# Optimization experiments

Hardware: AMD Instinct MI355X
Metric: run time of the kernel (lower is better)

Reference implementation:

```python
import jax, jax.numpy as jnp
import numpy as np

N, C_IN, NCLASS, H, W = 4, 32, 2, 64, 64


def setup_inputs() -> dict:
    key = jax.random.key(0)
    k1, k2, k3, k4, k5, k6 = jax.random.split(key, 6)
    return {
        "feature_in": jax.random.normal(k1, (N, C_IN, H, W), dtype=jnp.float32),
        "out": jax.random.normal(k2, (N, NCLASS, H, W), dtype=jnp.float32),
        "w1": jax.random.normal(k3, (NCLASS, C_IN), dtype=jnp.float32) * 0.1,
        "b1": jax.random.normal(k4, (NCLASS,), dtype=jnp.float32) * 0.1,
        "w2": jax.random.normal(k5, (NCLASS, C_IN), dtype=jnp.float32) * 0.1,
        "b2": jax.random.normal(k6, (NCLASS,), dtype=jnp.float32) * 0.1,
    }


def reference(feature_in, out, w1, b1, w2, b2):
    # h_in, w_in == input H, W (ceil(H/1)); bilinear resize to the same size
    # with align_corners=True is an exact identity, so no resampling is needed.
    n, c, h, w = feature_in.shape
    hw = h * w
    out = jax.lax.stop_gradient(out)  # out.detach() in the original

    # 1x1 convs == per-pixel linear projections
    f1 = jnp.einsum('nchw,kc->nkhw', feature_in, w1) + b1[None, :, None, None]
    f2 = jnp.einsum('nchw,kc->nkhw', feature_in, w2) + b2[None, :, None, None]
    f1 = f1.reshape(n, -1, hw)          # n k (h w)
    f2 = f2.reshape(n, -1, hw)
    out_flat = out.reshape(n, -1, hw)   # n c (h w)

    scale = 1.0 / jnp.sqrt(jnp.float32(f1.shape[1]))
    corr_map = jnp.einsum('nkp,nkq->npq', f1, f2) * scale  # [n, hw, hw]
    corr_map = jax.nn.softmax(corr_map, axis=-1)

    o = jnp.einsum('ncp,npq->ncq', out_flat, corr_map)
    return o.reshape(n, -1, h, w)
```

## Files before the change

### kernel.cpp

```cpp
#include <hip/hip_runtime.h>

#define HW   4096
#define CIN  32
#define SCALE2 (0.70710678118654752f * 1.44269504088896340f)

__device__ __forceinline__ float exp2_raw(float x) {
#if __has_builtin(__builtin_amdgcn_exp2f)
    return __builtin_amdgcn_exp2f(x);
#else
    float r;
    asm("v_exp_f32 %0, %1" : "=v"(r) : "v"(x));
    return r;
#endif
}

__global__ __launch_bounds__(256) void proj_kernel(
        const float* __restrict__ feat,
        const float* __restrict__ w1, const float* __restrict__ b1,
        const float* __restrict__ w2, const float* __restrict__ b2,
        float2* __restrict__ f1v, float2* __restrict__ f2v) {
    __shared__ float4 red[4][64];
    int tid = threadIdx.x;
    int pl = tid & 63;
    int cq = tid >> 6;
    int b = blockIdx.x;
    int n = b >> 6;
    int p = ((b & 63) << 6) + pl;
    const float* fbase = feat + ((size_t)n * CIN + cq * 8) * HW + p;
    float a10 = 0.f, a11 = 0.f, a20 = 0.f, a21 = 0.f;
#pragma unroll
    for (int c = 0; c < 8; ++c) {
        float v = fbase[(size_t)c * HW];
        a10 += v * w1[cq * 8 + c];
        a11 += v * w1[32 + cq * 8 + c];
        a20 += v * w2[cq * 8 + c];
        a21 += v * w2[32 + cq * 8 + c];
    }
    red[cq][pl] = make_float4(a10, a11, a20, a21);
    __syncthreads();
    if (tid < 64) {
        float4 r0 = red[0][tid], r1 = red[1][tid], r2 = red[2][tid], r3 = red[3][tid];
        int idx = n * HW + ((b & 63) << 6) + tid;
        f1v[idx] = make_float2(r0.x + r1.x + r2.x + r3.x + b1[0],
                               r0.y + r1.y + r2.y + r3.y + b1[1]);
        f2v[idx] = make_float2(r0.z + r1.z + r2.z + r3.z + b2[0],
                               r0.w + r1.w + r2.w + r3.w + b2[1]);
    }
}

__global__ __launch_bounds__(256, 8) void rowstats_kernel(
        const float2* __restrict__ f1v, const float2* __restrict__ f2v,
        const float* __restrict__ outv, float4* __restrict__ stats4) {
    __shared__ float red[4][8];
    int tid = threadIdx.x;
    int lane = tid & 63;
    int wid = tid >> 6;
    int b = blockIdx.x;
    int n = b >> 9;
    int pg = (b & 511) << 3;
    int base = n * HW;

    float f10[8], f11[8];
#pragma unroll
    for (int j = 0; j < 8; ++j) {
        float2 f1 = f1v[base + pg + j];
        f10[j] = f1.x * SCALE2;
        f11[j] = f1.y * SCALE2;
    }
    const float4* f2b = (const float4*)(f2v + base) + wid * 512 + lane;
    float acc[8];
#pragma unroll
    for (int j = 0; j < 8; ++j) acc[j] = 0.f;
#pragma unroll 2
    for (int s = 0; s < 8; ++s) {
        float4 ab = f2b[s * 64];
#pragma unroll
        for (int j = 0; j < 8; ++j) {
            float e0 = exp2_raw(f10[j] * ab.x + f11[j] * ab.y);
            float e1 = exp2_raw(f10[j] * ab.z + f11[j] * ab.w);
            acc[j] += e0 + e1;
        }
    }
#pragma unroll
    for (int j = 0; j < 8; ++j) {
        float a = acc[j];
        a += __shfl_xor(a, 1);  a += __shfl_xor(a, 2);
        a += __shfl_xor(a, 4);  a += __shfl_xor(a, 8);
        a += __shfl_xor(a, 16); a += __shfl_xor(a, 32);
        acc[j] = a;
    }
    if (lane == 0) {
#pragma unroll
        for (int j = 0; j < 8; ++j) red[wid][j] = acc[j];
    }
    __syncthreads();
    if (tid < 8) {
        float lt = red[0][tid] + red[1][tid] + red[2][tid] + red[3][tid];
        float inv = 1.0f / lt;
        int pp = pg + tid;
        float2 f1 = f1v[base + pp];
        float v0 = outv[(n * 2 + 0) * HW + pp];
        float v1 = outv[(n * 2 + 1) * HW + pp];
        stats4[base + pp] = make_float4(f1.x * SCALE2, f1.y * SCALE2, v0 * inv, v1 * inv);
    }
}

__global__ __launch_bounds__(256, 8) void colout_kernel(
        const float2* __restrict__ f2v, const float4* __restrict__ stats4,
        float* __restrict__ o) {
    __shared__ float red[4][8][2];
    int tid = threadIdx.x;
    int lane = tid & 63;
    int wid = tid >> 6;
    int b = blockIdx.x;
    int n = b >> 9;
    int qg = (b & 511) << 3;
    int base = n * HW;

    float g0[8], g1[8];
#pragma unroll
    for (int j = 0; j < 8; ++j) {
        float2 f2 = f2v[base + qg + j];
        g0[j] = f2.x;
        g1[j] = f2.y;
    }
    const float4* stb = stats4 + base + wid * 1024 + lane;
    float o0[8], o1[8];
#pragma unroll
    for (int j = 0; j < 8; ++j) { o0[j] = 0.f; o1[j] = 0.f; }
#pragma unroll 2
    for (int s = 0; s < 16; ++s) {
        float4 st = stb[s * 64];
#pragma unroll
        for (int j = 0; j < 8; ++j) {
            float e = exp2_raw(g0[j] * st.x + g1[j] * st.y);
            o0[j] += st.z * e;
            o1[j] += st.w * e;
        }
    }
#pragma unroll
    for (int j = 0; j < 8; ++j) {
        float a = o0[j], c = o1[j];
        a += __shfl_xor(a, 1);  c += __shfl_xor(c, 1);
        a += __shfl_xor(a, 2);  c += __shfl_xor(c, 2);
        a += __shfl_xor(a, 4);  c += __shfl_xor(c, 4);
        a += __shfl_xor(a, 8);  c += __shfl_xor(c, 8);
        a += __shfl_xor(a, 16); c += __shfl_xor(c, 16);
        a += __shfl_xor(a, 32); c += __shfl_xor(c, 32);
        o0[j] = a; o1[j] = c;
    }
    if (lane == 0) {
#pragma unroll
        for (int j = 0; j < 8; ++j) { red[wid][j][0] = o0[j]; red[wid][j][1] = o1[j]; }
    }
    __syncthreads();
    if (tid < 16) {
        int qq = tid >> 1, c = tid & 1;
        float r = red[0][qq][c] + red[1][qq][c] + red[2][qq][c] + red[3][qq][c];
        o[(n * 2 + c) * HW + qg + qq] = r;
    }
}

extern "C" void kernel_launch(void* const* d_in, const int* in_sizes, int n_in,
                              void* d_out, int out_size, void* d_ws, size_t ws_size,
                              hipStream_t stream) {
    const float* feat = (const float*)d_in[0];
    const float* outv = (const float*)d_in[1];
    const float* w1   = (const float*)d_in[2];
    const float* b1   = (const float*)d_in[3];
    const float* w2   = (const float*)d_in[4];
    const float* b2   = (const float*)d_in[5];
    float* o = (float*)d_out;

    float*  ws     = (float*)d_ws;
    float2* f1v    = (float2*)ws;
    float2* f2v    = (float2*)(ws + 32768);
    float4* stats4 = (float4*)(ws + 65536);

    proj_kernel<<<256, 256, 0, stream>>>(feat, w1, b1, w2, b2, f1v, f2v);
    rowstats_kernel<<<2048, 256, 0, stream>>>(f1v, f2v, outv, stats4);
    colout_kernel<<<2048, 256, 0, stream>>>(f2v, stats4, o);
}
```

Before: 35.67 us.

## Double rows per block, prefetch column tiles, use scalar loads for row operands

Each block in the rowstats and colout kernels now handles 16 rows or columns instead of 8, so the grid is halved and each loaded f2/stats element is reused across twice as many exponentials. The inner loop is fully unrolled with a one-step register prefetch of the next tile. Row operands are addressed through a readfirstlane-uniform index so they can come from scalar loads. The cost is more registers per thread (launch bounds relaxed from 8 waves), which may reduce occupancy.

Measured after the change: 35.53 us. About the same (-0.4%).

```diff
diff --git a/kernel.cpp b/kernel.cpp
--- a/kernel.cpp
+++ b/kernel.cpp
@@ -48,41 +48,44 @@
     }
 }
 
-__global__ __launch_bounds__(256, 8) void rowstats_kernel(
+__global__ __launch_bounds__(256) void rowstats_kernel(
         const float2* __restrict__ f1v, const float2* __restrict__ f2v,
         const float* __restrict__ outv, float4* __restrict__ stats4) {
-    __shared__ float red[4][8];
+    __shared__ float red[4][16];
     int tid = threadIdx.x;
     int lane = tid & 63;
     int wid = tid >> 6;
     int b = blockIdx.x;
-    int n = b >> 9;
-    int pg = (b & 511) << 3;
+    int n = b >> 8;
+    int pg = (b & 255) << 4;
     int base = n * HW;
 
-    float f10[8], f11[8];
+    int ub = __builtin_amdgcn_readfirstlane(base + pg);
+    float f10[16], f11[16];
 #pragma unroll
-    for (int j = 0; j < 8; ++j) {
-        float2 f1 = f1v[base + pg + j];
+    for (int j = 0; j < 16; ++j) {
+        float2 f1 = f1v[ub + j];
         f10[j] = f1.x * SCALE2;
         f11[j] = f1.y * SCALE2;
     }
     const float4* f2b = (const float4*)(f2v + base) + wid * 512 + lane;
-    float acc[8];
+    float acc[16];
 #pragma unroll
-    for (int j = 0; j < 8; ++j) acc[j] = 0.f;
-#pragma unroll 2
+    for (int j = 0; j < 16; ++j) acc[j] = 0.f;
+    float4 cur = f2b[0];
+#pragma unroll
     for (int s = 0; s < 8; ++s) {
-        float4 ab = f2b[s * 64];
+        float4 nxt = f2b[((s + 1) & 7) * 64];
 #pragma unroll
-        for (int j = 0; j < 8; ++j) {
-            float e0 = exp2_raw(f10[j] * ab.x + f11[j] * ab.y);
-            float e1 = exp2_raw(f10[j] * ab.z + f11[j] * ab.w);
+        for (int j = 0; j < 16; ++j) {
+            float e0 = exp2_raw(f10[j] * cur.x + f11[j] * cur.y);
+            float e1 = exp2_raw(f10[j] * cur.z + f11[j] * cur.w);
             acc[j] += e0 + e1;
         }
+        cur = nxt;
     }
 #pragma unroll
-    for (int j = 0; j < 8; ++j) {
+    for (int j = 0; j < 16; ++j) {
         float a = acc[j];
         a += __shfl_xor(a, 1);  a += __shfl_xor(a, 2);
         a += __shfl_xor(a, 4);  a += __shfl_xor(a, 8);
@@ -91,10 +94,10 @@
     }
     if (lane == 0) {
 #pragma unroll
-        for (int j = 0; j < 8; ++j) red[wid][j] = acc[j];
+        for (int j = 0; j < 16; ++j) red[wid][j] = acc[j];
     }
     __syncthreads();
-    if (tid < 8) {
+    if (tid < 16) {
         float lt = red[0][tid] + red[1][tid] + red[2][tid] + red[3][tid];
         float inv = 1.0f / lt;
         int pp = pg + tid;
@@ -105,41 +108,44 @@
     }
 }
 
-__global__ __launch_bounds__(256, 8) void colout_kernel(
+__global__ __launch_bounds__(256) void colout_kernel(
         const float2* __restrict__ f2v, const float4* __restrict__ stats4,
         float* __restrict__ o) {
-    __shared__ float red[4][8][2];
+    __shared__ float red[4][16][2];
     int tid = threadIdx.x;
     int lane = tid & 63;
     int wid = tid >> 6;
     int b = blockIdx.x;
-    int n = b >> 9;
-    int qg = (b & 511) << 3;
+    int n = b >> 8;
+    int qg = (b & 255) << 4;
     int base = n * HW;
 
-    float g0[8], g1[8];
+    int ub = __builtin_amdgcn_readfirstlane(base + qg);
+    float g0[16], g1[16];
 #pragma unroll
-    for (int j = 0; j < 8; ++j) {
-        float2 f2 = f2v[base + qg + j];
+    for (int j = 0; j < 16; ++j) {
+        float2 f2 = f2v[ub + j];
         g0[j] = f2.x;
         g1[j] = f2.y;
     }
     const float4* stb = stats4 + base + wid * 1024 + lane;
-    float o0[8], o1[8];
+    float o0[16], o1[16];
 #pragma unroll
-    for (int j = 0; j < 8; ++j) { o0[j] = 0.f; o1[j] = 0.f; }
-#pragma unroll 2
+    for (int j = 0; j < 16; ++j) { o0[j] = 0.f; o1[j] = 0.f; }
+    float4 cur = stb[0];
+#pragma unroll
     for (int s = 0; s < 16; ++s) {
-        float4 st = stb[s * 64];
+        float4 nxt = stb[((s + 1) & 15) * 64];
 #pragma unroll
-        for (int j = 0; j < 8; ++j) {
-            float e = exp2_raw(g0[j] * st.x + g1[j] * st.y);
-            o0[j] += st.z * e;
-            o1[j] += st.w * e;
+        for (int j = 0; j < 16; ++j) {
+            float e = exp2_raw(g0[j] * cur.x + g1[j] * cur.y);
+            o0[j] += cur.z * e;
+            o1[j] += cur.w * e;
         }
+        cur = nxt;
     }
 #pragma unroll
-    for (int j = 0; j < 8; ++j) {
+    for (int j = 0; j < 16; ++j) {
         float a = o0[j], c = o1[j];
         a += __shfl_xor(a, 1);  c += __shfl_xor(c, 1);
         a += __shfl_xor(a, 2);  c += __shfl_xor(c, 2);
@@ -151,10 +157,10 @@
     }
     if (lane == 0) {
 #pragma unroll
-        for (int j = 0; j < 8; ++j) { red[wid][j][0] = o0[j]; red[wid][j][1] = o1[j]; }
+        for (int j = 0; j < 16; ++j) { red[wid][j][0] = o0[j]; red[wid][j][1] = o1[j]; }
     }
     __syncthreads();
-    if (tid < 16) {
+    if (tid < 32) {
         int qq = tid >> 1, c = tid & 1;
         float r = red[0][qq][c] + red[1][qq][c] + red[2][qq][c] + red[3][qq][c];
         o[(n * 2 + c) * HW + qg + qq] = r;
@@ -178,6 +184,6 @@
     float4* stats4 = (float4*)(ws + 65536);
 
     proj_kernel<<<256, 256, 0, stream>>>(feat, w1, b1, w2, b2, f1v, f2v);
-    rowstats_kernel<<<2048, 256, 0, stream>>>(f1v, f2v, outv, stats4);
-    colout_kernel<<<2048, 256, 0, stream>>>(f2v, stats4, o);
+    rowstats_kernel<<<1024, 256, 0, stream>>>(f1v, f2v, outv, stats4);
+    colout_kernel<<<1024, 256, 0, stream>>>(f2v, stats4, o);
 }
```
